# Kernel tuning notes

Hardware: AMD Instinct MI355X
Metric: run time of the kernel (lower is better)

The kernel has to match this reference:

```python
import jax, jax.numpy as jnp
import numpy as np
import math

NUM_CLASSES = 80
MAX_ANCHOR_MATCHES = 10
ALPHA = 0.5
BETA = 6.0
EPSILON = 1e-9        # label-encoder epsilon
KEPS = 1e-7           # keras.backend.epsilon() used inside compute_ciou
B, NB = 16, 64        # batch, padded max GT boxes


def make_anchor_points():
    # YOLOv8 @ 640x640: strides 8/16/32 -> 80^2 + 40^2 + 20^2 = 8400 anchors
    pts = []
    for stride, n in [(8, 80), (16, 40), (32, 20)]:
        xs = (jnp.arange(n, dtype=jnp.float32) + 0.5) * stride
        gy, gx = jnp.meshgrid(xs, xs, indexing='ij')
        pts.append(jnp.stack([gx.reshape(-1), gy.reshape(-1)], axis=-1))
    return jnp.concatenate(pts, axis=0)  # (8400, 2)


def setup_inputs() -> dict:
    key = jax.random.key(0)
    k0, k1, k2, k3, k4, k5 = jax.random.split(key, 6)
    anc_points = make_anchor_points()
    NA = anc_points.shape[0]
    pd_scores = jax.random.uniform(k0, (B, NA, NUM_CLASSES), dtype=jnp.float32)
    # predicted boxes roughly centered on anchors
    wh = jax.random.uniform(k1, (B, NA, 2), minval=8.0, maxval=96.0)
    ctr = anc_points[None] + jax.random.normal(k2, (B, NA, 2)) * 8.0
    pd_bboxes = jnp.concatenate([ctr - wh / 2, ctr + wh / 2], axis=-1)
    # ground-truth boxes (xyxy) inside a 640x640 image
    g_wh = jax.random.uniform(k3, (B, NB, 2), minval=16.0, maxval=200.0)
    g_ctr = jax.random.uniform(k4, (B, NB, 2), minval=40.0, maxval=600.0)
    gt_bboxes = jnp.concatenate([g_ctr - g_wh / 2, g_ctr + g_wh / 2], axis=-1)
    gt_labels = jax.random.randint(k5, (B, NB), 0, NUM_CLASSES).astype(jnp.float32)
    # first 48 of 64 padded slots are real boxes
    mask_gt = jnp.broadcast_to(jnp.arange(NB)[None, :, None] < 48, (B, NB, 1))
    return {
        'pd_scores': pd_scores,
        'pd_bboxes': pd_bboxes,
        'anc_points': anc_points,
        'gt_labels': gt_labels,
        'gt_bboxes': gt_bboxes,
        'mask_gt': mask_gt,
    }


def compute_ciou(b1, b2):
    """CIoU between xyxy boxes b1 (gt) and b2 (pred); broadcasts, returns (...,)."""
    x1a, y1a, x2a, y2a = b1[..., 0], b1[..., 1], b1[..., 2], b1[..., 3]
    x1b, y1b, x2b, y2b = b2[..., 0], b2[..., 1], b2[..., 2], b2[..., 3]
    w1 = x2a - x1a
    h1 = y2a - y1a + KEPS
    w2 = x2b - x1b
    h2 = y2b - y1b + KEPS
    inter = (jnp.maximum(jnp.minimum(x2a, x2b) - jnp.maximum(x1a, x1b), 0.0)
             * jnp.maximum(jnp.minimum(y2a, y2b) - jnp.maximum(y1a, y1b), 0.0))
    union = w1 * h1 + w2 * h2 - inter + KEPS
    iou = inter / union
    cw = jnp.maximum(x2a, x2b) - jnp.minimum(x1a, x1b)
    ch = jnp.maximum(y2a, y2b) - jnp.minimum(y1a, y1b)
    c2 = cw * cw + ch * ch + KEPS
    rho2 = ((x1a + x2a) / 2 - (x1b + x2b) / 2) ** 2 + ((y1a + y2a) / 2 - (y1b + y2b) / 2) ** 2
    v = (4.0 / math.pi ** 2) * (jnp.arctan(w2 / h2) - jnp.arctan(w1 / h1)) ** 2
    alpha = v / (v - iou + (1.0 + KEPS))
    return iou - (rho2 / c2 + v * alpha)


def _encode(pd_scores, pd_bboxes, anc_points, gt_labels, gt_bboxes, mask_gt):
    Bn, NA, NC = pd_scores.shape
    NBn = gt_bboxes.shape[1]
    f32 = pd_scores.dtype
    mask_gt_b = mask_gt.astype(bool)                      # (B, NB, 1)

    # --- select_candidates_in_gts: anchor center inside gt box ---
    lt = gt_bboxes[:, :, None, :2]                        # (B, NB, 1, 2)
    rb = gt_bboxes[:, :, None, 2:]
    anc = anc_points[None, None, :, :]                    # (1, 1, NA, 2)
    deltas = jnp.concatenate([anc - lt, rb - anc], -1)    # (B, NB, NA, 4)
    mask_in_gts = jnp.min(deltas, axis=-1) > EPSILON      # (B, NB, NA)
    valid = mask_in_gts & mask_gt_b                       # (B, NB, NA)

    # --- get_box_metrics ---
    lbl = jnp.maximum(gt_labels.astype(jnp.int32), 0)     # (B, NB)
    sc = jnp.take_along_axis(pd_scores, jnp.broadcast_to(lbl[:, None, :], (Bn, NA, NBn)), axis=-1)
    sc = jnp.transpose(sc, (0, 2, 1))                     # (B, NB, NA)
    sc = jnp.where(gt_labels[:, :, None] >= 0, sc, 0.0)
    bbox_scores = jnp.where(valid, sc, 0.0)
    iou = compute_ciou(gt_bboxes[:, :, None, :], pd_bboxes[:, None, :, :])  # (B, NB, NA)
    iou = jnp.where(iou > 0, iou, 0.0)
    overlaps = jnp.where(valid, iou, 0.0)
    align_metric = jnp.power(bbox_scores, ALPHA) * jnp.power(overlaps, BETA)

    # --- select_topk_candidates ---
    k = MAX_ANCHOR_MATCHES
    _, topk_idxs = jax.lax.top_k(align_metric, k)         # (B, NB, k)
    topk_idxs = jnp.where(jnp.broadcast_to(mask_gt_b, (Bn, NBn, k)), topk_idxs, 0)
    bi = jnp.arange(Bn)[:, None, None]
    gi = jnp.arange(NBn)[None, :, None]
    counts = jnp.zeros((Bn, NBn, NA), f32).at[bi, gi, topk_idxs].add(1.0)
    mask_topk = jnp.where(counts > 1, 0.0, counts)        # drop idx-0 duplicates
    mask_pos = mask_topk * mask_in_gts.astype(f32) * mask_gt_b.astype(f32)

    # --- select_highest_overlaps (tie-break anchors matched to >1 gt) ---
    fg_mask = jnp.sum(mask_pos, axis=-2)                  # (B, NA)
    mask_multi = jnp.broadcast_to((fg_mask > 1)[:, None, :], (Bn, NBn, NA))
    max_idx = jnp.argmax(overlaps, axis=1)                # (B, NA)
    is_max = jnp.transpose(jax.nn.one_hot(max_idx, NBn, dtype=f32), (0, 2, 1))
    mask_pos = jnp.where(mask_multi, is_max, mask_pos)
    fg_mask = jnp.sum(mask_pos, axis=-2)
    target_gt_idx = jnp.argmax(mask_pos, axis=-2)         # (B, NA)

    # --- get_targets ---
    target_labels = jnp.take_along_axis(lbl, target_gt_idx, axis=1)          # (B, NA)
    target_bboxes = jnp.take_along_axis(gt_bboxes, target_gt_idx[..., None], axis=1)  # (B, NA, 4)
    target_scores = jax.nn.one_hot(target_labels, NC, dtype=f32)
    target_scores = jnp.where((fg_mask > 0)[..., None], target_scores, 0.0)

    # --- normalize class targets by alignment metric ---
    align_metric = align_metric * mask_pos
    pos_align = jnp.max(align_metric, axis=-1, keepdims=True)                # (B, NB, 1)
    pos_overlaps = jnp.max(overlaps * mask_pos, axis=-1, keepdims=True)
    norm = jnp.max(align_metric * pos_overlaps / (pos_align + EPSILON), axis=-2)[..., None]
    target_scores = target_scores * norm
    return target_bboxes, target_scores, fg_mask


def reference(pd_scores, pd_bboxes, anc_points, gt_labels, gt_bboxes, mask_gt):
    tb, ts, fg = _encode(pd_scores, pd_bboxes, anc_points, gt_labels, gt_bboxes, mask_gt)
    return (jax.lax.stop_gradient(tb), jax.lax.stop_gradient(ts), jax.lax.stop_gradient(fg))
```

## Files before the change

### kernel.cpp

```cpp
#include <hip/hip_runtime.h>
#include <cstdint>
#include <cstddef>

#define NBg 64
#define NCg 80
#define KTOP 10
#define K16 16
#define CAPW 1024

typedef unsigned long long u64k;

__device__ __forceinline__ float ciou_dev(float gx1, float gy1, float gx2, float gy2,
                                          float px1, float py1, float px2, float py2) {
#pragma clang fp contract(off)
  const float keps = 1e-7f;
  float w1 = gx2 - gx1;
  float h1 = (gy2 - gy1) + keps;
  float w2 = px2 - px1;
  float h2 = (py2 - py1) + keps;
  float iw = fminf(gx2, px2) - fmaxf(gx1, px1);
  float ih = fminf(gy2, py2) - fmaxf(gy1, py1);
  float inter = fmaxf(iw, 0.0f) * fmaxf(ih, 0.0f);
  float uni = w1 * h1 + w2 * h2 - inter + keps;
  float iou = inter / uni;
  float cw = fmaxf(gx2, px2) - fminf(gx1, px1);
  float ch = fmaxf(gy2, py2) - fminf(gy1, py1);
  float c2 = cw * cw + ch * ch + keps;
  float dx = (gx1 + gx2) * 0.5f - (px1 + px2) * 0.5f;
  float dy = (gy1 + gy2) * 0.5f - (py1 + py2) * 0.5f;
  float rho2 = dx * dx + dy * dy;
  float q2 = w2 / h2;
  float q1 = w1 / h1;
  float t = (float)atan((double)q2) - (float)atan((double)q1);
  float v = 0.4052847345693511f * (t * t);
  float alpha = v / ((v - iou) + 1.0000001f);
  return iou - (rho2 / c2 + v * alpha);
}

__device__ __forceinline__ float am_dev(float sc, float ov) {
  float f1 = (float)sqrt((double)sc);
  double o = (double)ov;
  double o3 = o * o * o;
  return f1 * (float)(o3 * o3);
}

__device__ __forceinline__ u64k mk_key(float am, int a) {
  return ((u64k)__float_as_uint(am) << 32) | (unsigned)(~a);
}

__device__ __forceinline__ void merge16(u64k (&L)[K16], const u64k (&B)[K16]) {
  u64k C[K16];
#pragma unroll
  for (int i = 0; i < K16; i++) {
    u64k x = L[i], y = B[15 - i];
    C[i] = x > y ? x : y;
  }
#pragma unroll
  for (int s = 8; s > 0; s >>= 1) {
#pragma unroll
    for (int i = 0; i < K16; i++) {
      if ((i & s) == 0) {
        u64k x = C[i], y = C[i | s];
        C[i] = x > y ? x : y;
        C[i | s] = x > y ? y : x;
      }
    }
  }
#pragma unroll
  for (int i = 0; i < K16; i++) L[i] = C[i];
}

__global__ void ka_topk(const float* __restrict__ pd_scores,
                        const float* __restrict__ pd_bboxes,
                        const float* __restrict__ anc,
                        const float* __restrict__ gt_labels,
                        const float* __restrict__ gt_bboxes,
                        const int* __restrict__ mask_gt,
                        int* __restrict__ sel,
                        float* __restrict__ posAlign,
                        float* __restrict__ posOv,
                        int NA) {
  int row = blockIdx.x;
  int tid = threadIdx.x;
  int lane = tid & 63;
  int wid = tid >> 6;
  if (tid == 0) { posAlign[row] = 0.0f; posOv[row] = 0.0f; }
  if (!mask_gt[row]) {
    if (tid < KTOP) sel[row * KTOP + tid] = -1;
    return;
  }
  int b = row >> 6;
  const float* g = gt_bboxes + (size_t)row * 4;
  float gx1 = g[0], gy1 = g[1], gx2 = g[2], gy2 = g[3];
  float gl = gt_labels[row];
  int lbl = gl > 0.0f ? (int)gl : 0;
  bool glpos = (gl >= 0.0f);
  const float2* anc2 = (const float2*)anc;

  __shared__ int slist[4 * CAPW];
  __shared__ u64k xl[4][K16];

  u64k k[KTOP];
#pragma unroll
  for (int q = 0; q < KTOP; q++) k[q] = 0;

  auto ins = [&](u64k key) {
    if (key > k[KTOP - 1]) {
      k[KTOP - 1] = key;
#pragma unroll
      for (int q = KTOP - 1; q > 0; q--) {
        if (k[q] > k[q - 1]) { u64k t = k[q]; k[q] = k[q - 1]; k[q - 1] = t; }
      }
    }
  };

  auto heavy = [&](int a) {
    const float4 pb = ((const float4*)pd_bboxes)[(size_t)b * NA + a];
    float ci = ciou_dev(gx1, gy1, gx2, gy2, pb.x, pb.y, pb.z, pb.w);
    float ov = ci > 0.0f ? ci : 0.0f;
    float sc = glpos ? pd_scores[((size_t)b * NA + a) * NCg + lbl] : 0.0f;
    ins(mk_key(am_dev(sc, ov), a));
  };

  int wcnt = 0;
  u64k lmask_lt = (1ull << lane) - 1;
#pragma unroll
  for (int itb = 0; itb < 9; itb++) {
    float2 p[4];
    int idx[4];
#pragma unroll
    for (int u = 0; u < 4; u++) {
      idx[u] = tid + (itb * 4 + u) * 256;
      p[u] = (idx[u] < NA) ? anc2[idx[u]] : make_float2(0.0f, 0.0f);
    }
#pragma unroll
    for (int u = 0; u < 4; u++) {
      bool valid = idx[u] < NA;
      float dmin = fminf(fminf(p[u].x - gx1, p[u].y - gy1),
                         fminf(gx2 - p[u].x, gy2 - p[u].y));
      bool inbox = valid && (dmin > 1e-9f);
      u64k m = __ballot(inbox);
      if (inbox) {
        int pos = wcnt + __popcll(m & lmask_lt);
        if (pos < CAPW) slist[wid * CAPW + pos] = idx[u];
        else heavy(idx[u]);
      } else if (valid) {
        ins((u64k)(unsigned)(~idx[u]));
      }
      wcnt += __popcll(m);
    }
  }
  int wslots = wcnt < CAPW ? wcnt : CAPW;

  for (int i = lane; i < wslots; i += 64) heavy(slist[wid * CAPW + i]);

  u64k L[K16];
#pragma unroll
  for (int q = 0; q < KTOP; q++) L[q] = k[q];
#pragma unroll
  for (int q = KTOP; q < K16; q++) L[q] = 0;

#pragma unroll
  for (int step = 0; step < 6; step++) {
    u64k B[K16];
#pragma unroll
    for (int q = 0; q < K16; q++)
      B[q] = __shfl_xor((unsigned long long)L[q], 1 << step, 64);
    merge16(L, B);
  }

  if (lane < K16) xl[wid][lane] = L[lane];
  __syncthreads();
  if (wid == 2) {
    u64k B[K16];
#pragma unroll
    for (int q = 0; q < K16; q++) B[q] = xl[3][q];
    merge16(L, B);
    if (lane < K16) xl[2][lane] = L[lane];
  }
  if (wid == 0) {
    u64k B[K16];
#pragma unroll
    for (int q = 0; q < K16; q++) B[q] = xl[1][q];
    merge16(L, B);
  }
  __syncthreads();
  if (wid == 0) {
    u64k B[K16];
#pragma unroll
    for (int q = 0; q < K16; q++) B[q] = xl[2][q];
    merge16(L, B);
    if (lane == 0) {
#pragma unroll
      for (int q = 0; q < KTOP; q++) {
        int a = ~((unsigned)L[q]);
        float2 ap = anc2[a];
        float dmin = fminf(fminf(ap.x - gx1, ap.y - gy1),
                           fminf(gx2 - ap.x, gy2 - ap.y));
        sel[row * KTOP + q] = (dmin > 1e-9f) ? a : -1;
      }
    }
  }
}

__global__ void k3_resolve(const float* __restrict__ pd_scores,
                           const float* __restrict__ pd_bboxes,
                           const float* __restrict__ anc,
                           const float* __restrict__ gt_labels,
                           const float* __restrict__ gt_bboxes,
                           const int* __restrict__ mask_gt,
                           const int* __restrict__ sel,
                           int* __restrict__ tgt,
                           float* __restrict__ amv,
                           float* __restrict__ out_tb,
                           float* __restrict__ out_fg,
                           float* __restrict__ posAlign,
                           float* __restrict__ posOv,
                           int NA) {
  int b = blockIdx.y;
  int tid = threadIdx.x;
  int a0 = blockIdx.x * 256;
  int a = a0 + tid;
  __shared__ float4 sg[NBg];
  __shared__ int svalid[NBg];
  __shared__ int slbl[NBg];
  __shared__ int sglpos[NBg];
  __shared__ unsigned int mlo[256];
  __shared__ unsigned int mhi[256];
  mlo[tid] = 0u; mhi[tid] = 0u;
  if (tid < NBg) {
    int j = tid;
    const float* g = gt_bboxes + ((size_t)b * NBg + j) * 4;
    sg[j] = make_float4(g[0], g[1], g[2], g[3]);
    svalid[j] = mask_gt[b * NBg + j];
    float gl = gt_labels[b * NBg + j];
    slbl[j] = gl > 0.0f ? (int)gl : 0;
    sglpos[j] = (gl >= 0.0f) ? 1 : 0;
  }
  __syncthreads();
  for (int i = tid; i < NBg * KTOP; i += 256) {
    int e = sel[b * NBg * KTOP + i];
    int d = e - a0;
    if (d >= 0 && d < 256) {
      int j = i / KTOP;
      unsigned int bit = 1u << (j & 31);
      if (j < 32) atomicOr(&mlo[d], bit); else atomicOr(&mhi[d], bit);
    }
  }
  __syncthreads();
  if (a >= NA) return;
  unsigned int lo = mlo[tid], hi = mhi[tid];
  int cnt = __popc(lo) + __popc(hi);
  int first = lo ? (__ffs(lo) - 1) : (hi ? 32 + __ffs(hi) - 1 : 0);

  float ax = anc[2 * a], ay = anc[2 * a + 1];
  float px1 = 0.f, py1 = 0.f, px2 = 0.f, py2 = 0.f;
  if (cnt > 0) {
    const float* pb = pd_bboxes + ((size_t)b * NA + a) * 4;
    px1 = pb[0]; py1 = pb[1]; px2 = pb[2]; py2 = pb[3];
  }
  int t = 0;
  float fg = 0.0f;
  float ovt = -1.0f;
  if (cnt == 1) {
    t = first; fg = 1.0f;
  } else if (cnt > 1) {
    float best = -1.0f;
    for (int jj = 0; jj < NBg; jj++) {
      float ov = 0.0f;
      if (svalid[jj]) {
        float4 g = sg[jj];
        float dmin = fminf(fminf(ax - g.x, ay - g.y), fminf(g.z - ax, g.w - ay));
        if (dmin > 1e-9f) {
          float ci = ciou_dev(g.x, g.y, g.z, g.w, px1, py1, px2, py2);
          ov = ci > 0.0f ? ci : 0.0f;
        }
      }
      if (ov > best) { best = ov; t = jj; }
    }
    fg = 1.0f;
    ovt = best;
  }
  tgt[(size_t)b * NA + a] = t;
  out_fg[(size_t)b * NA + a] = fg;
  float4 gb = sg[t];
  ((float4*)out_tb)[(size_t)b * NA + a] = gb;
  float amval = 0.0f;
  if (fg > 0.0f) {
    float ov;
    if (ovt >= 0.0f) {
      ov = ovt;
    } else {
      float ci = ciou_dev(gb.x, gb.y, gb.z, gb.w, px1, py1, px2, py2);
      ov = ci > 0.0f ? ci : 0.0f;
    }
    float sc = sglpos[t] ? pd_scores[((size_t)b * NA + a) * NCg + slbl[t]] : 0.0f;
    amval = am_dev(sc, ov);
    atomicMax((int*)(posAlign + b * NBg + t), __float_as_int(amval));
    atomicMax((int*)(posOv + b * NBg + t), __float_as_int(ov));
  }
  amv[(size_t)b * NA + a] = amval;
}

__global__ void k5_scores(const float* __restrict__ gt_labels,
                          const int* __restrict__ tgt,
                          const float* __restrict__ out_fg,
                          const float* __restrict__ amv,
                          const float* __restrict__ posAlign,
                          const float* __restrict__ posOv,
                          float* __restrict__ out_ts,
                          int NA) {
  int b = blockIdx.y;
  int a0 = blockIdx.x * 256;
  int tid = threadIdx.x;
  int a = a0 + tid;
  __shared__ float snorm[256];
  __shared__ int slab[256];
  float norm = 0.0f;
  int lbl = -1;
  if (a < NA) {
    int t = tgt[(size_t)b * NA + a];
    float fg = out_fg[(size_t)b * NA + a];
    if (fg > 0.0f) {
      float av = amv[(size_t)b * NA + a];
      norm = av * posOv[b * NBg + t] / (posAlign[b * NBg + t] + 1e-9f);
      float gl = gt_labels[b * NBg + t];
      lbl = gl > 0.0f ? (int)gl : 0;
    }
  }
  snorm[tid] = norm;
  slab[tid] = lbl;
  __syncthreads();
  int nanch = NA - a0; if (nanch > 256) nanch = 256;
  int nf4 = nanch * (NCg / 4);
  float4* o = (float4*)(out_ts + ((size_t)b * NA + a0) * NCg);
  for (int i = tid; i < nf4; i += 256) {
    int aa = i / (NCg / 4);
    int c0 = (i % (NCg / 4)) * 4;
    int lb = slab[aa];
    float nv = snorm[aa];
    float4 w = make_float4(0.0f, 0.0f, 0.0f, 0.0f);
    int d = lb - c0;
    if (d >= 0 && d < 4) ((float*)&w)[d] = nv;
    o[i] = w;
  }
}

extern "C" void kernel_launch(void* const* d_in, const int* in_sizes, int n_in,
                              void* d_out, int out_size, void* d_ws, size_t ws_size,
                              hipStream_t stream) {
  const float* pd_scores = (const float*)d_in[0];
  const float* pd_bboxes = (const float*)d_in[1];
  const float* anc       = (const float*)d_in[2];
  const float* gt_labels = (const float*)d_in[3];
  const float* gt_bboxes = (const float*)d_in[4];
  const int*   mask_gt   = (const int*)d_in[5];

  int NA = in_sizes[2] / 2;
  int B  = in_sizes[3] / NBg;
  size_t nBA = (size_t)B * NA;

  float* out_tb = (float*)d_out;
  float* out_ts = out_tb + nBA * 4;
  float* out_fg = out_ts + nBA * NCg;

  char* ws = (char*)d_ws;
  size_t off = 0;
  int* sel = (int*)(ws + off);                off += (size_t)B * NBg * KTOP * 4;
  int* tgt = (int*)(ws + off);                off += nBA * 4;
  float* amv = (float*)(ws + off);            off += nBA * 4;
  float* posAlign = (float*)(ws + off);       off += (size_t)B * NBg * 4;
  float* posOv = (float*)(ws + off);          off += (size_t)B * NBg * 4;

  dim3 blk(256);
  int rows = B * NBg;
  ka_topk<<<rows, blk, 0, stream>>>(pd_scores, pd_bboxes, anc, gt_labels,
                                    gt_bboxes, mask_gt, sel, posAlign, posOv, NA);
  dim3 gA((NA + 255) / 256, B);
  k3_resolve<<<gA, blk, 0, stream>>>(pd_scores, pd_bboxes, anc, gt_labels,
                                     gt_bboxes, mask_gt, sel, tgt, amv,
                                     out_tb, out_fg, posAlign, posOv, NA);
  k5_scores<<<gA, blk, 0, stream>>>(gt_labels, tgt, out_fg, amv, posAlign, posOv,
                                    out_ts, NA);
}
```

Before: 171.2 us.

## Scan only anchor grid cells overlapping each GT box instead of all anchors

```diff
diff --git a/kernel.cpp b/kernel.cpp
--- a/kernel.cpp
+++ b/kernel.cpp
@@ -6,7 +6,6 @@
 #define NCg 80
 #define KTOP 10
 #define K16 16
-#define CAPW 1024
 
 typedef unsigned long long u64k;
 
@@ -95,10 +94,23 @@
   float gl = gt_labels[row];
   int lbl = gl > 0.0f ? (int)gl : 0;
   bool glpos = (gl >= 0.0f);
-  const float2* anc2 = (const float2*)anc;
-
-  __shared__ int slist[4 * CAPW];
-  __shared__ u64k xl[4][K16];
+
+  auto rect = [&](float s, int n, int& x0, int& y0, int& w, int& h) {
+    int i0 = (int)floorf(gx1 / s - 0.5f) - 1; if (i0 < 0) i0 = 0;
+    int i1 = (int)ceilf (gx2 / s - 0.5f) + 1; if (i1 > n - 1) i1 = n - 1;
+    int j0 = (int)floorf(gy1 / s - 0.5f) - 1; if (j0 < 0) j0 = 0;
+    int j1 = (int)ceilf (gy2 / s - 0.5f) + 1; if (j1 > n - 1) j1 = n - 1;
+    x0 = i0; y0 = j0;
+    w = i1 - i0 + 1; h = j1 - j0 + 1;
+    if (w < 0) w = 0;
+    if (h < 0) h = 0;
+  };
+  int x00, y00, w0, h0, x01, y01, w1, h1, x02, y02, w2, h2;
+  rect( 8.0f, 80, x00, y00, w0, h0);
+  rect(16.0f, 40, x01, y01, w1, h1);
+  rect(32.0f, 20, x02, y02, w2, h2);
+  int sz0 = w0 * h0, sz1 = w1 * h1, sz2 = w2 * h2;
+  int tot = sz0 + sz1 + sz2;
 
   u64k k[KTOP];
 #pragma unroll
@@ -114,45 +126,25 @@
     }
   };
 
-  auto heavy = [&](int a) {
-    const float4 pb = ((const float4*)pd_bboxes)[(size_t)b * NA + a];
-    float ci = ciou_dev(gx1, gy1, gx2, gy2, pb.x, pb.y, pb.z, pb.w);
-    float ov = ci > 0.0f ? ci : 0.0f;
-    float sc = glpos ? pd_scores[((size_t)b * NA + a) * NCg + lbl] : 0.0f;
-    ins(mk_key(am_dev(sc, ov), a));
-  };
-
-  int wcnt = 0;
-  u64k lmask_lt = (1ull << lane) - 1;
-#pragma unroll
-  for (int itb = 0; itb < 9; itb++) {
-    float2 p[4];
-    int idx[4];
-#pragma unroll
-    for (int u = 0; u < 4; u++) {
-      idx[u] = tid + (itb * 4 + u) * 256;
-      p[u] = (idx[u] < NA) ? anc2[idx[u]] : make_float2(0.0f, 0.0f);
-    }
-#pragma unroll
-    for (int u = 0; u < 4; u++) {
-      bool valid = idx[u] < NA;
-      float dmin = fminf(fminf(p[u].x - gx1, p[u].y - gy1),
-                         fminf(gx2 - p[u].x, gy2 - p[u].y));
-      bool inbox = valid && (dmin > 1e-9f);
-      u64k m = __ballot(inbox);
-      if (inbox) {
-        int pos = wcnt + __popcll(m & lmask_lt);
-        if (pos < CAPW) slist[wid * CAPW + pos] = idx[u];
-        else heavy(idx[u]);
-      } else if (valid) {
-        ins((u64k)(unsigned)(~idx[u]));
-      }
-      wcnt += __popcll(m);
-    }
-  }
-  int wslots = wcnt < CAPW ? wcnt : CAPW;
-
-  for (int i = lane; i < wslots; i += 64) heavy(slist[wid * CAPW + i]);
+  for (int c = tid; c < tot; c += 256) {
+    int cc, x0, y0, w, nbase, ngrid; float ss;
+    if (c < sz0)              { cc = c;              x0 = x00; y0 = y00; w = w0; nbase = 0;    ngrid = 80; ss =  8.0f; }
+    else if (c < sz0 + sz1)   { cc = c - sz0;        x0 = x01; y0 = y01; w = w1; nbase = 6400; ngrid = 40; ss = 16.0f; }
+    else                      { cc = c - sz0 - sz1;  x0 = x02; y0 = y02; w = w2; nbase = 8000; ngrid = 20; ss = 32.0f; }
+    int iy = y0 + cc / w;
+    int ix = x0 + cc % w;
+    float ax = ((float)ix + 0.5f) * ss;
+    float ay = ((float)iy + 0.5f) * ss;
+    float dmin = fminf(fminf(ax - gx1, ay - gy1), fminf(gx2 - ax, gy2 - ay));
+    if (dmin > 1e-9f) {
+      int a = nbase + iy * ngrid + ix;
+      const float4 pb = ((const float4*)pd_bboxes)[(size_t)b * NA + a];
+      float ci = ciou_dev(gx1, gy1, gx2, gy2, pb.x, pb.y, pb.z, pb.w);
+      float ov = ci > 0.0f ? ci : 0.0f;
+      float sc = glpos ? pd_scores[((size_t)b * NA + a) * NCg + lbl] : 0.0f;
+      ins(mk_key(am_dev(sc, ov), a));
+    }
+  }
 
   u64k L[K16];
 #pragma unroll
@@ -169,6 +161,7 @@
     merge16(L, B);
   }
 
+  __shared__ u64k xl[4][K16];
   if (lane < K16) xl[wid][lane] = L[lane];
   __syncthreads();
   if (wid == 2) {
@@ -191,13 +184,29 @@
     for (int q = 0; q < K16; q++) B[q] = xl[2][q];
     merge16(L, B);
     if (lane == 0) {
-#pragma unroll
-      for (int q = 0; q < KTOP; q++) {
-        int a = ~((unsigned)L[q]);
+      int npos = 0;
+#pragma unroll
+      for (int q = 0; q < KTOP; q++) if ((L[q] >> 32) != 0) npos++;
+      int cand = 0;
+      const float2* anc2 = (const float2*)anc;
+      for (int slot = 0; slot < KTOP; slot++) {
+        int a;
+        if (slot < npos) {
+          a = (int)~(unsigned)L[slot];
+        } else {
+          bool moved = true;
+          while (moved) {
+            moved = false;
+#pragma unroll
+            for (int q = 0; q < KTOP; q++)
+              if (q < npos && (int)~(unsigned)L[q] == cand) { cand++; moved = true; }
+          }
+          a = cand++;
+        }
         float2 ap = anc2[a];
         float dmin = fminf(fminf(ap.x - gx1, ap.y - gy1),
                            fminf(gx2 - ap.x, gy2 - ap.y));
-        sel[row * KTOP + q] = (dmin > 1e-9f) ? a : -1;
+        sel[row * KTOP + slot] = (dmin > 1e-9f) ? a : -1;
       }
     }
   }
@@ -265,18 +274,28 @@
   if (cnt == 1) {
     t = first; fg = 1.0f;
   } else if (cnt > 1) {
-    float best = -1.0f;
+    unsigned bm_lo = 0u, bm_hi = 0u;
     for (int jj = 0; jj < NBg; jj++) {
-      float ov = 0.0f;
       if (svalid[jj]) {
-        float4 g = sg[jj];
-        float dmin = fminf(fminf(ax - g.x, ay - g.y), fminf(g.z - ax, g.w - ay));
+        float4 gq = sg[jj];
+        float dmin = fminf(fminf(ax - gq.x, ay - gq.y), fminf(gq.z - ax, gq.w - ay));
         if (dmin > 1e-9f) {
-          float ci = ciou_dev(g.x, g.y, g.z, g.w, px1, py1, px2, py2);
-          ov = ci > 0.0f ? ci : 0.0f;
+          if (jj < 32) bm_lo |= 1u << jj; else bm_hi |= 1u << (jj - 32);
         }
       }
-      if (ov > best) { best = ov; t = jj; }
+    }
+    float best = 0.0f;
+    t = 0;
+    unsigned m = bm_lo; int base = 0;
+    for (int half = 0; half < 2; half++) {
+      while (m) {
+        int jj = base + __ffs(m) - 1; m &= m - 1;
+        float4 gq = sg[jj];
+        float ci = ciou_dev(gq.x, gq.y, gq.z, gq.w, px1, py1, px2, py2);
+        float ov = ci > 0.0f ? ci : 0.0f;
+        if (ov > best) { best = ov; t = jj; }
+      }
+      m = bm_hi; base = 32;
     }
     fg = 1.0f;
     ovt = best;
```

Measured after the change: 158.4 us. -7.5%, faster.
